# Kernel tuning notes

Hardware: AMD Instinct MI355X
Metric: run time of the kernel (lower is better)

The kernel has to match this reference:

```python
import jax, jax.numpy as jnp
import numpy as np

EPS = 1e-10
COMMITMENT_COST = 0.25


def setup_inputs() -> dict:
    key = jax.random.key(0)
    k1, k2, k3, k4 = jax.random.split(key, 4)
    return {
        "x": jax.random.normal(k1, (32, 64, 64, 64), dtype=jnp.float32),  # NCHW, C=D=64
        "emb0": jax.random.normal(k2, (512, 64), dtype=jnp.float32),
        "emb1": jax.random.normal(k3, (512, 64), dtype=jnp.float32),
        "emb2": jax.random.normal(k4, (512, 64), dtype=jnp.float32),
        "idx": 1,
    }


def reference(x, emb0, emb1, emb2, idx):
    # NCHW -> NHWC, flatten to [N, D]
    inputs = jnp.transpose(x, (0, 2, 3, 1))
    in_shape = inputs.shape
    D = in_shape[-1]
    flat = inputs.reshape(-1, D)  # [N, D]

    if idx == 0:
        codes = emb0
    elif idx == 1:
        codes = jnp.concatenate([emb0, emb1], axis=0)
    else:
        codes = jnp.concatenate([emb0, emb2], axis=0)  # [K, D]

    distances = (
        jnp.sum(flat * flat, axis=1, keepdims=True)
        + jnp.sum(codes * codes, axis=1)
        - 2.0 * jnp.matmul(flat, codes.T)
    )
    enc_idx = jnp.argmin(distances, axis=1)  # [N]

    # one-hot @ codes is just a gather
    quantized = codes[enc_idx].reshape(in_shape)

    e_latent_loss = jnp.mean((jax.lax.stop_gradient(quantized) - inputs) ** 2)
    q_latent_loss = jnp.mean((quantized - jax.lax.stop_gradient(inputs)) ** 2)
    loss = q_latent_loss + COMMITMENT_COST * e_latent_loss

    # straight-through estimator
    quantized_st = inputs + jax.lax.stop_gradient(quantized - inputs)

    K = codes.shape[0]
    N = flat.shape[0]
    avg_probs = jnp.zeros((K,), dtype=flat.dtype).at[enc_idx].add(1.0) / N
    perplexity = jnp.exp(-jnp.sum(avg_probs * jnp.log(avg_probs + EPS)))

    return jnp.transpose(quantized_st, (0, 3, 1, 2)), loss, perplexity
```

## Files before the change

kernel.cpp:

```cpp
#include <hip/hip_runtime.h>
#include <math.h>

#define NROWS   131072
#define DFEAT   64
#define KHALF   512
#define HW      4096
#define CHW     262144
#define NQOUT   8388608

typedef __attribute__((ext_vector_type(8))) short   bf16x8;
typedef __attribute__((ext_vector_type(4))) float   f32x4;

__device__ __forceinline__ unsigned short f2bf(float f) {
    unsigned int u = __float_as_uint(f);
    u += 0x7FFFu + ((u >> 16) & 1u);
    return (unsigned short)(u >> 16);
}
__device__ __forceinline__ float bf2f(unsigned short h) {
    return __uint_as_float(((unsigned int)h) << 16);
}

__global__ void vq_cnorm(const float* __restrict__ e0, const float* __restrict__ e1,
                         const float* __restrict__ e2, const int* __restrict__ idxp,
                         float* __restrict__ cnh) {
    int k = blockIdx.x * blockDim.x + threadIdx.x;
    if (k >= 1024) return;
    int idx = idxp[0];
    const float* sel = (idx == 2) ? e2 : e1;
    const float* row = (k < KHALF) ? (e0 + (size_t)k * DFEAT)
                                   : (sel + (size_t)(k - KHALF) * DFEAT);
    float s = 0.f;
#pragma unroll
    for (int c = 0; c < DFEAT; ++c) s = fmaf(row[c], row[c], s);
    cnh[k] = 0.5f * s;
}

__global__ void vq_pack(const float* __restrict__ e0, const float* __restrict__ e1,
                        const float* __restrict__ e2, const int* __restrict__ idxp,
                        unsigned short* __restrict__ fragbuf) {
    int tau = blockIdx.x * 256 + threadIdx.x;
    int tile = tau >> 8;
    int rem  = tau & 255;
    int f    = rem >> 6;
    int L    = rem & 63;
    int code = tile * 16 + (L & 15);
    int kb   = (f & 1) * 32 + (L >> 4) * 8;
    int lo_f = f >> 1;
    int idx  = idxp[0];
    const float* sel = (idx == 2) ? e2 : e1;
    const float* src = (code < KHALF) ? (e0 + (size_t)code * DFEAT)
                                      : (sel + (size_t)(code - KHALF) * DFEAT);
    unsigned short* dst = fragbuf + (size_t)tau * 8;
#pragma unroll
    for (int j = 0; j < 8; ++j) {
        float v = src[kb + j];
        unsigned short hb = f2bf(v);
        dst[j] = lo_f ? f2bf(v - bf2f(hb)) : hb;
    }
}

__global__ __launch_bounds__(256, 2) void vq_main(
        const float* __restrict__ x,
        const float* __restrict__ e0, const float* __restrict__ e1,
        const float* __restrict__ e2, const int* __restrict__ idxp,
        const float* __restrict__ cnh, const unsigned short* __restrict__ fragbuf,
        float* __restrict__ out, float* __restrict__ loss_acc,
        int* __restrict__ hist) {
    __shared__ float xsq_s[256];
    __shared__ float sc_s[256];
    __shared__ int   bk_s[256];

    const int t = threadIdx.x;
    const int w = t >> 6;
    const int L = t & 63;
    const int q = L >> 4;
    const int m = L & 15;

    const int rowbase = blockIdx.x * 256;
    const int n  = rowbase >> 12;
    const int s0 = rowbase & 4095;

    const int idx = idxp[0];
    const float* sel = (idx == 2) ? e2 : e1;
    const int ntiles = (idx == 0) ? 32 : 64;

    bf16x8 ahi[4][2], alo[4][2];
    const float* xb = x + (size_t)n * CHW + (s0 + w * 64);
#pragma unroll
    for (int rt = 0; rt < 4; ++rt) {
        const float* xr = xb + rt * 16 + m;
        float xs = 0.f;
#pragma unroll
        for (int h = 0; h < 2; ++h) {
#pragma unroll
            for (int j = 0; j < 8; ++j) {
                int c = h * 32 + q * 8 + j;
                float v = xr[(size_t)c * HW];
                xs = fmaf(v, v, xs);
                unsigned short hb = f2bf(v);
                unsigned short lb = f2bf(v - bf2f(hb));
                ahi[rt][h][j] = (short)hb;
                alo[rt][h][j] = (short)lb;
            }
        }
        xs += __shfl_xor(xs, 16, 64);
        xs += __shfl_xor(xs, 32, 64);
        if (q == 0) xsq_s[w * 64 + rt * 16 + m] = xs;
    }

    const bf16x8* fb = (const bf16x8*)fragbuf;
    float best[16];
    int   bidx[16];
#pragma unroll
    for (int i = 0; i < 16; ++i) { best[i] = -3.4e38f; bidx[i] = 0; }

    bf16x8 bc0 = fb[0 * 64 + L];
    bf16x8 bc1 = fb[1 * 64 + L];
    bf16x8 bc2 = fb[2 * 64 + L];
    bf16x8 bc3 = fb[3 * 64 + L];
    float  cnc = cnh[m];

    for (int tt = 0; tt < ntiles; ++tt) {
        const int tn = (tt + 1 < ntiles) ? tt + 1 : tt;
        bf16x8 bn0 = fb[(tn * 4 + 0) * 64 + L];
        bf16x8 bn1 = fb[(tn * 4 + 1) * 64 + L];
        bf16x8 bn2 = fb[(tn * 4 + 2) * 64 + L];
        bf16x8 bn3 = fb[(tn * 4 + 3) * 64 + L];
        float  cnn = cnh[tn * 16 + m];
        const int kt = tt * 16 + m;
#pragma unroll
        for (int rt = 0; rt < 4; ++rt) {
            f32x4 acc = {0.f, 0.f, 0.f, 0.f};
            acc = __builtin_amdgcn_mfma_f32_16x16x32_bf16(ahi[rt][0], bc0, acc, 0, 0, 0);
            acc = __builtin_amdgcn_mfma_f32_16x16x32_bf16(ahi[rt][1], bc1, acc, 0, 0, 0);
            acc = __builtin_amdgcn_mfma_f32_16x16x32_bf16(ahi[rt][0], bc2, acc, 0, 0, 0);
            acc = __builtin_amdgcn_mfma_f32_16x16x32_bf16(ahi[rt][1], bc3, acc, 0, 0, 0);
            acc = __builtin_amdgcn_mfma_f32_16x16x32_bf16(alo[rt][0], bc0, acc, 0, 0, 0);
            acc = __builtin_amdgcn_mfma_f32_16x16x32_bf16(alo[rt][1], bc1, acc, 0, 0, 0);
            acc = __builtin_amdgcn_mfma_f32_16x16x32_bf16(alo[rt][0], bc2, acc, 0, 0, 0);
            acc = __builtin_amdgcn_mfma_f32_16x16x32_bf16(alo[rt][1], bc3, acc, 0, 0, 0);
#pragma unroll
            for (int r = 0; r < 4; ++r) {
                float s = acc[r] - cnc;
                if (s > best[rt * 4 + r]) { best[rt * 4 + r] = s; bidx[rt * 4 + r] = kt; }
            }
        }
        bc0 = bn0; bc1 = bn1; bc2 = bn2; bc3 = bn3; cnc = cnn;
    }

#pragma unroll
    for (int i = 0; i < 16; ++i) {
        float b = best[i]; int k = bidx[i];
#pragma unroll
        for (int off = 1; off < 16; off <<= 1) {
            float ob = __shfl_xor(b, off, 64);
            int   ok = __shfl_xor(k, off, 64);
            if (ob > b || (ob == b && ok < k)) { b = ob; k = ok; }
        }
        if (m == 0) {
            int row = w * 64 + (i >> 2) * 16 + q * 4 + (i & 3);
            sc_s[row] = b; bk_s[row] = k;
        }
    }
    __syncthreads();

    const int k   = bk_s[t];
    float dist    = xsq_s[t] - 2.f * sc_s[t];
    float l = dist;
#pragma unroll
    for (int off = 32; off > 0; off >>= 1) l += __shfl_down(l, off, 64);
    if (L == 0) atomicAdd(loss_acc, l);
    atomicAdd(&hist[k], 1);

    const float* cp = (k < KHALF) ? (e0 + (size_t)k * DFEAT)
                                  : (sel + (size_t)(k - KHALF) * DFEAT);
    const float4* cp4 = (const float4*)cp;
    float* op = out + (size_t)n * CHW + (s0 + t);
#pragma unroll
    for (int c4 = 0; c4 < 16; ++c4) {
        float4 v = cp4[c4];
        op[(size_t)(4 * c4 + 0) * HW] = v.x;
        op[(size_t)(4 * c4 + 1) * HW] = v.y;
        op[(size_t)(4 * c4 + 2) * HW] = v.z;
        op[(size_t)(4 * c4 + 3) * HW] = v.w;
    }
}

__global__ void vq_finalize(const float* __restrict__ wsf, const int* __restrict__ hist,
                            float* __restrict__ out) {
    __shared__ double partial[16];
    const int t = threadIdx.x;
    double p = (double)hist[t] / (double)NROWS;
    double term = p * log(p + 1e-10);
#pragma unroll
    for (int off = 32; off > 0; off >>= 1) term += __shfl_down(term, off, 64);
    if ((t & 63) == 0) partial[t >> 6] = term;
    __syncthreads();
    if (t == 0) {
        double s = 0.0;
        for (int i = 0; i < 16; ++i) s += partial[i];
        out[NQOUT + 1] = (float)exp(-s);
        out[NQOUT]     = 1.25f * (wsf[0] / (float)NQOUT);
    }
}

extern "C" void kernel_launch(void* const* d_in, const int* in_sizes, int n_in,
                              void* d_out, int out_size, void* d_ws, size_t ws_size,
                              hipStream_t stream) {
    const float* x  = (const float*)d_in[0];
    const float* e0 = (const float*)d_in[1];
    const float* e1 = (const float*)d_in[2];
    const float* e2 = (const float*)d_in[3];
    const int* idxp = (const int*)d_in[4];
    float* out = (float*)d_out;

    float* wsf      = (float*)d_ws;
    float* loss_acc = wsf;
    int*   hist     = (int*)(wsf + 256);
    float* cnh      = wsf + 2048;
    unsigned short* fragbuf = (unsigned short*)(wsf + 4096);

    hipMemsetAsync(d_ws, 0, 1280 * sizeof(float), stream);
    vq_cnorm<<<4, 256, 0, stream>>>(e0, e1, e2, idxp, cnh);
    vq_pack<<<64, 256, 0, stream>>>(e0, e1, e2, idxp, fragbuf);
    vq_main<<<NROWS / 256, 256, 0, stream>>>(x, e0, e1, e2, idxp, cnh, fragbuf,
                                             out, loss_acc, hist);
    vq_finalize<<<1, 1024, 0, stream>>>(wsf, hist, out);
}
```

Before: 194.1 us.

## Fuse prep kernels, finalize in last block, halve rows per block, drop lo*lo MFMAs

Merges the codebook norm, pack and workspace-zeroing steps into one prep kernel, replacing the memset. The finalize kernel becomes a last-block-done epilogue in the main kernel, using an atomic counter. Each main block now handles 128 rows instead of 256, doubling the block count, and launch bounds allow 4 blocks per CU. The two alo×blo MFMAs per tile are also dropped, cutting matrix work by a quarter at some precision cost, which could flip argmin ties. The perplexity reduction moves from double to float.

```diff
diff --git a/kernel.cpp b/kernel.cpp
--- a/kernel.cpp
+++ b/kernel.cpp
@@ -7,6 +7,7 @@
 #define HW      4096
 #define CHW     262144
 #define NQOUT   8388608
+#define MAIN_BLOCKS 1024
 
 typedef __attribute__((ext_vector_type(8))) short   bf16x8;
 typedef __attribute__((ext_vector_type(4))) float   f32x4;
@@ -20,55 +21,62 @@
     return __uint_as_float(((unsigned int)h) << 16);
 }
 
-__global__ void vq_cnorm(const float* __restrict__ e0, const float* __restrict__ e1,
-                         const float* __restrict__ e2, const int* __restrict__ idxp,
-                         float* __restrict__ cnh) {
-    int k = blockIdx.x * blockDim.x + threadIdx.x;
-    if (k >= 1024) return;
-    int idx = idxp[0];
+__global__ void vq_prep(const float* __restrict__ e0, const float* __restrict__ e1,
+                        const float* __restrict__ e2, const int* __restrict__ idxp,
+                        unsigned short* __restrict__ fragbuf, float* __restrict__ cnh,
+                        int* __restrict__ hist, float* __restrict__ loss_acc,
+                        int* __restrict__ done) {
+    const int tau = blockIdx.x * 256 + threadIdx.x;
+    const int idx = idxp[0];
     const float* sel = (idx == 2) ? e2 : e1;
-    const float* row = (k < KHALF) ? (e0 + (size_t)k * DFEAT)
-                                   : (sel + (size_t)(k - KHALF) * DFEAT);
-    float s = 0.f;
-#pragma unroll
-    for (int c = 0; c < DFEAT; ++c) s = fmaf(row[c], row[c], s);
-    cnh[k] = 0.5f * s;
-}
-
-__global__ void vq_pack(const float* __restrict__ e0, const float* __restrict__ e1,
-                        const float* __restrict__ e2, const int* __restrict__ idxp,
-                        unsigned short* __restrict__ fragbuf) {
-    int tau = blockIdx.x * 256 + threadIdx.x;
-    int tile = tau >> 8;
-    int rem  = tau & 255;
-    int f    = rem >> 6;
-    int L    = rem & 63;
-    int code = tile * 16 + (L & 15);
-    int kb   = (f & 1) * 32 + (L >> 4) * 8;
-    int lo_f = f >> 1;
-    int idx  = idxp[0];
-    const float* sel = (idx == 2) ? e2 : e1;
-    const float* src = (code < KHALF) ? (e0 + (size_t)code * DFEAT)
-                                      : (sel + (size_t)(code - KHALF) * DFEAT);
-    unsigned short* dst = fragbuf + (size_t)tau * 8;
-#pragma unroll
-    for (int j = 0; j < 8; ++j) {
-        float v = src[kb + j];
-        unsigned short hb = f2bf(v);
-        dst[j] = lo_f ? f2bf(v - bf2f(hb)) : hb;
-    }
-}
-
-__global__ __launch_bounds__(256, 2) void vq_main(
+
+    {
+        int tile = tau >> 8;
+        int rem  = tau & 255;
+        int f    = rem >> 6;
+        int L    = rem & 63;
+        int code = tile * 16 + (L & 15);
+        int kb   = (f & 1) * 32 + (L >> 4) * 8;
+        int lo_f = f >> 1;
+        const float* src = (code < KHALF) ? (e0 + (size_t)code * DFEAT)
+                                          : (sel + (size_t)(code - KHALF) * DFEAT);
+        unsigned short* dst = fragbuf + (size_t)tau * 8;
+#pragma unroll
+        for (int j = 0; j < 8; ++j) {
+            float v = src[kb + j];
+            unsigned short hb = f2bf(v);
+            dst[j] = lo_f ? f2bf(v - bf2f(hb)) : hb;
+        }
+    }
+
+    if (tau < 1024) {
+        const float* row = (tau < KHALF) ? (e0 + (size_t)tau * DFEAT)
+                                         : (sel + (size_t)(tau - KHALF) * DFEAT);
+        float s = 0.f;
+#pragma unroll
+        for (int c = 0; c < DFEAT; ++c) s = fmaf(row[c], row[c], s);
+        cnh[tau] = 0.5f * s;
+    }
+
+    if (blockIdx.x == 0) {
+#pragma unroll
+        for (int i = 0; i < 4; ++i) hist[threadIdx.x * 4 + i] = 0;
+        if (threadIdx.x == 0) { loss_acc[0] = 0.f; done[0] = 0; }
+    }
+}
+
+__global__ __launch_bounds__(256, 4) void vq_main(
         const float* __restrict__ x,
         const float* __restrict__ e0, const float* __restrict__ e1,
         const float* __restrict__ e2, const int* __restrict__ idxp,
         const float* __restrict__ cnh, const unsigned short* __restrict__ fragbuf,
         float* __restrict__ out, float* __restrict__ loss_acc,
-        int* __restrict__ hist) {
-    __shared__ float xsq_s[256];
-    __shared__ float sc_s[256];
-    __shared__ int   bk_s[256];
+        int* __restrict__ hist, int* __restrict__ done) {
+    __shared__ float xsq_s[128];
+    __shared__ float sc_s[128];
+    __shared__ int   bk_s[128];
+    __shared__ float pf[4];
+    __shared__ int   lastflag;
 
     const int t = threadIdx.x;
     const int w = t >> 6;
@@ -76,7 +84,7 @@
     const int q = L >> 4;
     const int m = L & 15;
 
-    const int rowbase = blockIdx.x * 256;
+    const int rowbase = blockIdx.x * 128;
     const int n  = rowbase >> 12;
     const int s0 = rowbase & 4095;
 
@@ -84,10 +92,10 @@
     const float* sel = (idx == 2) ? e2 : e1;
     const int ntiles = (idx == 0) ? 32 : 64;
 
-    bf16x8 ahi[4][2], alo[4][2];
-    const float* xb = x + (size_t)n * CHW + (s0 + w * 64);
-#pragma unroll
-    for (int rt = 0; rt < 4; ++rt) {
+    bf16x8 ahi[2][2], alo[2][2];
+    const float* xb = x + (size_t)n * CHW + (s0 + w * 32);
+#pragma unroll
+    for (int rt = 0; rt < 2; ++rt) {
         const float* xr = xb + rt * 16 + m;
         float xs = 0.f;
 #pragma unroll
@@ -105,51 +113,49 @@
         }
         xs += __shfl_xor(xs, 16, 64);
         xs += __shfl_xor(xs, 32, 64);
-        if (q == 0) xsq_s[w * 64 + rt * 16 + m] = xs;
+        if (q == 0) xsq_s[w * 32 + rt * 16 + m] = xs;
     }
 
     const bf16x8* fb = (const bf16x8*)fragbuf;
-    float best[16];
-    int   bidx[16];
-#pragma unroll
-    for (int i = 0; i < 16; ++i) { best[i] = -3.4e38f; bidx[i] = 0; }
-
-    bf16x8 bc0 = fb[0 * 64 + L];
-    bf16x8 bc1 = fb[1 * 64 + L];
-    bf16x8 bc2 = fb[2 * 64 + L];
-    bf16x8 bc3 = fb[3 * 64 + L];
+    float best[8];
+    int   bidx[8];
+#pragma unroll
+    for (int i = 0; i < 8; ++i) { best[i] = -3.4e38f; bidx[i] = 0; }
+
+    bf16x8 bh0 = fb[0 * 64 + L];
+    bf16x8 bh1 = fb[1 * 64 + L];
+    bf16x8 bl0 = fb[2 * 64 + L];
+    bf16x8 bl1 = fb[3 * 64 + L];
     float  cnc = cnh[m];
 
     for (int tt = 0; tt < ntiles; ++tt) {
         const int tn = (tt + 1 < ntiles) ? tt + 1 : tt;
-        bf16x8 bn0 = fb[(tn * 4 + 0) * 64 + L];
-        bf16x8 bn1 = fb[(tn * 4 + 1) * 64 + L];
-        bf16x8 bn2 = fb[(tn * 4 + 2) * 64 + L];
-        bf16x8 bn3 = fb[(tn * 4 + 3) * 64 + L];
+        bf16x8 nh0 = fb[(tn * 4 + 0) * 64 + L];
+        bf16x8 nh1 = fb[(tn * 4 + 1) * 64 + L];
+        bf16x8 nl0 = fb[(tn * 4 + 2) * 64 + L];
+        bf16x8 nl1 = fb[(tn * 4 + 3) * 64 + L];
         float  cnn = cnh[tn * 16 + m];
         const int kt = tt * 16 + m;
 #pragma unroll
-        for (int rt = 0; rt < 4; ++rt) {
+        for (int rt = 0; rt < 2; ++rt) {
             f32x4 acc = {0.f, 0.f, 0.f, 0.f};
-            acc = __builtin_amdgcn_mfma_f32_16x16x32_bf16(ahi[rt][0], bc0, acc, 0, 0, 0);
-            acc = __builtin_amdgcn_mfma_f32_16x16x32_bf16(ahi[rt][1], bc1, acc, 0, 0, 0);
-            acc = __builtin_amdgcn_mfma_f32_16x16x32_bf16(ahi[rt][0], bc2, acc, 0, 0, 0);
-            acc = __builtin_amdgcn_mfma_f32_16x16x32_bf16(ahi[rt][1], bc3, acc, 0, 0, 0);
-            acc = __builtin_amdgcn_mfma_f32_16x16x32_bf16(alo[rt][0], bc0, acc, 0, 0, 0);
-            acc = __builtin_amdgcn_mfma_f32_16x16x32_bf16(alo[rt][1], bc1, acc, 0, 0, 0);
-            acc = __builtin_amdgcn_mfma_f32_16x16x32_bf16(alo[rt][0], bc2, acc, 0, 0, 0);
-            acc = __builtin_amdgcn_mfma_f32_16x16x32_bf16(alo[rt][1], bc3, acc, 0, 0, 0);
+            acc = __builtin_amdgcn_mfma_f32_16x16x32_bf16(ahi[rt][0], bh0, acc, 0, 0, 0);
+            acc = __builtin_amdgcn_mfma_f32_16x16x32_bf16(ahi[rt][1], bh1, acc, 0, 0, 0);
+            acc = __builtin_amdgcn_mfma_f32_16x16x32_bf16(ahi[rt][0], bl0, acc, 0, 0, 0);
+            acc = __builtin_amdgcn_mfma_f32_16x16x32_bf16(ahi[rt][1], bl1, acc, 0, 0, 0);
+            acc = __builtin_amdgcn_mfma_f32_16x16x32_bf16(alo[rt][0], bh0, acc, 0, 0, 0);
+            acc = __builtin_amdgcn_mfma_f32_16x16x32_bf16(alo[rt][1], bh1, acc, 0, 0, 0);
 #pragma unroll
             for (int r = 0; r < 4; ++r) {
                 float s = acc[r] - cnc;
                 if (s > best[rt * 4 + r]) { best[rt * 4 + r] = s; bidx[rt * 4 + r] = kt; }
             }
         }
-        bc0 = bn0; bc1 = bn1; bc2 = bn2; bc3 = bn3; cnc = cnn;
-    }
-
-#pragma unroll
-    for (int i = 0; i < 16; ++i) {
+        bh0 = nh0; bh1 = nh1; bl0 = nl0; bl1 = nl1; cnc = cnn;
+    }
+
+#pragma unroll
+    for (int i = 0; i < 8; ++i) {
         float b = best[i]; int k = bidx[i];
 #pragma unroll
         for (int off = 1; off < 16; off <<= 1) {
@@ -158,49 +164,58 @@
             if (ob > b || (ob == b && ok < k)) { b = ob; k = ok; }
         }
         if (m == 0) {
-            int row = w * 64 + (i >> 2) * 16 + q * 4 + (i & 3);
+            int row = w * 32 + (i >> 2) * 16 + q * 4 + (i & 3);
             sc_s[row] = b; bk_s[row] = k;
         }
     }
     __syncthreads();
 
-    const int k   = bk_s[t];
-    float dist    = xsq_s[t] - 2.f * sc_s[t];
-    float l = dist;
-#pragma unroll
-    for (int off = 32; off > 0; off >>= 1) l += __shfl_down(l, off, 64);
-    if (L == 0) atomicAdd(loss_acc, l);
-    atomicAdd(&hist[k], 1);
-
-    const float* cp = (k < KHALF) ? (e0 + (size_t)k * DFEAT)
-                                  : (sel + (size_t)(k - KHALF) * DFEAT);
-    const float4* cp4 = (const float4*)cp;
-    float* op = out + (size_t)n * CHW + (s0 + t);
-#pragma unroll
-    for (int c4 = 0; c4 < 16; ++c4) {
-        float4 v = cp4[c4];
-        op[(size_t)(4 * c4 + 0) * HW] = v.x;
-        op[(size_t)(4 * c4 + 1) * HW] = v.y;
-        op[(size_t)(4 * c4 + 2) * HW] = v.z;
-        op[(size_t)(4 * c4 + 3) * HW] = v.w;
-    }
-}
-
-__global__ void vq_finalize(const float* __restrict__ wsf, const int* __restrict__ hist,
-                            float* __restrict__ out) {
-    __shared__ double partial[16];
-    const int t = threadIdx.x;
-    double p = (double)hist[t] / (double)NROWS;
-    double term = p * log(p + 1e-10);
+    {
+        const int r  = t & 127;
+        const int h2 = t >> 7;
+        const int k  = bk_s[r];
+        float l = (h2 == 0) ? (xsq_s[r] - 2.f * sc_s[r]) : 0.f;
+#pragma unroll
+        for (int off = 32; off > 0; off >>= 1) l += __shfl_down(l, off, 64);
+        if (L == 0 && w < 2) atomicAdd(loss_acc, l);
+        if (h2 == 0) atomicAdd(&hist[k], 1);
+
+        const float* cp = (k < KHALF) ? (e0 + (size_t)k * DFEAT)
+                                      : (sel + (size_t)(k - KHALF) * DFEAT);
+        const float4* cp4 = (const float4*)(cp + h2 * 32);
+        float* op = out + (size_t)n * CHW + (size_t)h2 * 32 * HW + (s0 + r);
+#pragma unroll
+        for (int c4 = 0; c4 < 8; ++c4) {
+            float4 v = cp4[c4];
+            op[(size_t)(4 * c4 + 0) * HW] = v.x;
+            op[(size_t)(4 * c4 + 1) * HW] = v.y;
+            op[(size_t)(4 * c4 + 2) * HW] = v.z;
+            op[(size_t)(4 * c4 + 3) * HW] = v.w;
+        }
+    }
+
+    __threadfence();
+    __syncthreads();
+    if (t == 0) lastflag = (atomicAdd(done, 1) == MAIN_BLOCKS - 1);
+    __syncthreads();
+    if (!lastflag) return;
+
+    float term = 0.f;
+#pragma unroll
+    for (int i = 0; i < 4; ++i) {
+        int h = atomicAdd(&hist[t * 4 + i], 0);
+        float p = (float)h / (float)NROWS;
+        term += p * logf(p + 1e-10f);
+    }
 #pragma unroll
     for (int off = 32; off > 0; off >>= 1) term += __shfl_down(term, off, 64);
-    if ((t & 63) == 0) partial[t >> 6] = term;
+    if (L == 0) pf[w] = term;
     __syncthreads();
     if (t == 0) {
-        double s = 0.0;
-        for (int i = 0; i < 16; ++i) s += partial[i];
-        out[NQOUT + 1] = (float)exp(-s);
-        out[NQOUT]     = 1.25f * (wsf[0] / (float)NQOUT);
+        float s = pf[0] + pf[1] + pf[2] + pf[3];
+        float lv = atomicAdd(loss_acc, 0.f);
+        out[NQOUT]     = 1.25f * (lv / (float)NQOUT);
+        out[NQOUT + 1] = expf(-s);
     }
 }
 
@@ -216,14 +231,12 @@
 
     float* wsf      = (float*)d_ws;
     float* loss_acc = wsf;
+    int*   done     = (int*)(wsf + 2);
     int*   hist     = (int*)(wsf + 256);
     float* cnh      = wsf + 2048;
     unsigned short* fragbuf = (unsigned short*)(wsf + 4096);
 
-    hipMemsetAsync(d_ws, 0, 1280 * sizeof(float), stream);
-    vq_cnorm<<<4, 256, 0, stream>>>(e0, e1, e2, idxp, cnh);
-    vq_pack<<<64, 256, 0, stream>>>(e0, e1, e2, idxp, fragbuf);
-    vq_main<<<NROWS / 256, 256, 0, stream>>>(x, e0, e1, e2, idxp, cnh, fragbuf,
-                                             out, loss_acc, hist);
-    vq_finalize<<<1, 1024, 0, stream>>>(wsf, hist, out);
-}
+    vq_prep<<<64, 256, 0, stream>>>(e0, e1, e2, idxp, fragbuf, cnh, hist, loss_acc, done);
+    vq_main<<<MAIN_BLOCKS, 256, 0, stream>>>(x, e0, e1, e2, idxp, cnh, fragbuf,
+                                             out, loss_acc, hist, done);
+}
```

Measured after the change: 273.5 us. 40.9% more time.
